# Kernel tuning notes

Hardware: AMD Instinct MI355X
Metric: run time of the kernel (lower is better)

Reference implementation:

```python
import jax, jax.numpy as jnp
import numpy as np

B, T, D_EMB, D_H = 4, 4096, 512, 64


def setup_inputs() -> dict:
    key = jax.random.key(0)
    ks = jax.random.split(key, 7)
    s_in = 1.0 / np.sqrt(D_EMB)
    return {
        "x": jax.random.normal(ks[0], (B, T, D_EMB), jnp.float32),
        "Wq_w": jax.random.normal(ks[1], (D_H, D_EMB), jnp.float32) * s_in,
        "Wq_b": jax.random.normal(ks[2], (D_H,), jnp.float32) * 0.02,
        "Wk_w": jax.random.normal(ks[3], (D_H, D_EMB), jnp.float32) * s_in,
        "Wk_b": jax.random.normal(ks[4], (D_H,), jnp.float32) * 0.02,
        "Wv_w": jax.random.normal(ks[5], (D_H, D_EMB), jnp.float32) * s_in,
        "Wv_b": jax.random.normal(ks[6], (D_H,), jnp.float32) * 0.02,
    }


def reference(x, Wq_w, Wq_b, Wk_w, Wk_b, Wv_w, Wv_b):
    # Q,K,V: [B,T,d_h] via torch.nn.Linear semantics (x @ W.T + b)
    Q = jnp.einsum("btc,hc->bth", x, Wq_w) + Wq_b
    K = jnp.einsum("btc,hc->bth", x, Wk_w) + Wk_b
    V = jnp.einsum("btc,hc->bth", x, Wv_w) + Wv_b
    # raw scores [B,T,T], causal mask, softmax, then post-softmax scale by sqrt(d_h)
    scores = jnp.einsum("bqh,bkh->bqk", Q, K)
    causal = jnp.tril(jnp.ones((T, T), dtype=bool))
    scores = jnp.where(causal, scores, -jnp.inf)
    alpha = jax.nn.softmax(scores, axis=-1) * jnp.sqrt(jnp.float32(D_H))
    return jnp.einsum("bqk,bkh->bqh", alpha, V)
```

## Files before the change

### kernel.cpp

```cpp
#include <hip/hip_runtime.h>
#include <hip/hip_fp16.h>
#include <math.h>

#define B 4
#define T 4096
#define DEMB 512
#define DH 64
#define NSPLIT 16
#define NPTILE 16
#define LOG2E 1.44269504088896340736f

typedef _Float16 f16;
typedef __attribute__((ext_vector_type(4))) _Float16 f16x4;
typedef __attribute__((ext_vector_type(8))) _Float16 f16x8;
typedef __attribute__((ext_vector_type(4))) float f32x4;

__global__ __launch_bounds__(256) void convert_w(
    const float* __restrict__ Wq, const float* __restrict__ Wk,
    const float* __restrict__ Wv, f16* __restrict__ Wf)
{
    const int idx = blockIdx.x * 256 + threadIdx.x;
    const int row = idx >> 9;
    const int k   = idx & 511;
    const float* W = row < 64 ? Wq : (row < 128 ? Wk : Wv);
    Wf[idx] = (f16)W[(row & 63) * DEMB + k];
}

__global__ __launch_bounds__(512) void proj_mfma(
    const float* __restrict__ x, const f16* __restrict__ Wfg,
    const float* __restrict__ bq, const float* __restrict__ bk,
    const float* __restrict__ bv,
    f16* __restrict__ Qf, f16* __restrict__ Kf, f16* __restrict__ Vt)
{
    __shared__ f16 xs[32][136];
    __shared__ f16 Ws[192][136];

    const int tid  = threadIdx.x;
    const int wv   = tid >> 6;
    const int lane = tid & 63;
    const int i16  = lane & 15;
    const int quad = lane >> 4;
    const int rg   = wv >> 2;
    const int nh   = wv & 3;
    const size_t r0 = (size_t)blockIdx.x * 32;

    f32x4 acc[3];
    const f32x4 zero = {0.f, 0.f, 0.f, 0.f};
#pragma unroll
    for (int n = 0; n < 3; ++n) acc[n] = zero;

    for (int cc = 0; cc < DEMB; cc += 128) {
        __syncthreads();
        {
            const int row = tid >> 4, g = tid & 15;
            const float4 a = *(const float4*)(x + (r0 + row) * DEMB + cc + g * 8);
            const float4 b = *(const float4*)(x + (r0 + row) * DEMB + cc + g * 8 + 4);
            f16x8 h = {(f16)a.x, (f16)a.y, (f16)a.z, (f16)a.w,
                       (f16)b.x, (f16)b.y, (f16)b.z, (f16)b.w};
            *(f16x8*)&xs[row][g * 8] = h;
        }
#pragma unroll
        for (int u = 0; u < 6; ++u) {
            const int idx = tid + 512 * u;
            const int row = idx >> 4, g = idx & 15;
            *(f16x8*)&Ws[row][g * 8] =
                *(const f16x8*)(Wfg + (size_t)row * DEMB + cc + g * 8);
        }
        __syncthreads();

#pragma unroll
        for (int kk = 0; kk < 4; ++kk) {
            const f16x8 af = *(const f16x8*)&xs[rg * 16 + i16][kk * 32 + quad * 8];
#pragma unroll
            for (int n = 0; n < 3; ++n) {
                const f16x8 bf = *(const f16x8*)&Ws[(nh * 3 + n) * 16 + i16][kk * 32 + quad * 8];
                acc[n] = __builtin_amdgcn_mfma_f32_16x16x32_f16(af, bf, acc[n], 0, 0, 0);
            }
        }
    }

    const size_t bb = r0 / T;
    const size_t t0 = r0 - bb * T;
#pragma unroll
    for (int n = 0; n < 3; ++n) {
        const int col = (nh * 3 + n) * 16 + i16;
        const int m = col >> 6, h = col & 63;
        const float bias = (m == 0 ? bq : (m == 1 ? bk : bv))[h];
#pragma unroll
        for (int r = 0; r < 4; ++r) {
            const int row = rg * 16 + quad * 4 + r;
            const float v = acc[n][r] + bias;
            const size_t grow = r0 + row;
            if (m == 0)      Qf[grow * DH + h] = (f16)(v * LOG2E);
            else if (m == 1) Kf[grow * DH + h] = (f16)v;
            else             Vt[(bb * DH + h) * T + t0 + row] = (f16)v;
        }
    }
}

__global__ __launch_bounds__(512, 4) void attn_partial(
    const f16* __restrict__ Qf, const f16* __restrict__ Kf,
    const f16* __restrict__ Vt,
    f16* __restrict__ Opart, float* __restrict__ mpart,
    float* __restrict__ lpart)
{
    __shared__ f16 Ks[64][72], Vs[64][72];
    __shared__ f16 Pl[8][16][72];

    const int tid  = threadIdx.x;
    const int wv   = tid >> 6;
    const int lane = tid & 63;
    const int i16  = lane & 15;
    const int quad = lane >> 4;

    const int s    = blockIdx.x & 15;
    const int p    = 15 - ((blockIdx.x >> 4) & 15);
    const int bb   = blockIdx.x >> 8;
    const size_t base = (size_t)bb * T;
    const int row0 = p * 256;
    const int cmax = 4 * p + 3;
    const int rowg0 = row0 + wv * 16;
    const int rowg1 = row0 + (wv + 8) * 16;

    f16x8 qf00, qf01, qf10, qf11;
    {
        const f16* q0 = Qf + (base + rowg0 + i16) * DH;
        const f16* q1 = Qf + (base + rowg1 + i16) * DH;
        qf00 = *(const f16x8*)(q0 + quad * 8);
        qf01 = *(const f16x8*)(q0 + 32 + quad * 8);
        qf10 = *(const f16x8*)(q1 + quad * 8);
        qf11 = *(const f16x8*)(q1 + 32 + quad * 8);
    }

    f32x4 oacc[2][4];
    float mm[2] = {-INFINITY, -INFINITY}, ll[2] = {0.f, 0.f};
    const f32x4 zero = {0.f, 0.f, 0.f, 0.f};
#pragma unroll
    for (int j = 0; j < 2; ++j)
#pragma unroll
        for (int n = 0; n < 4; ++n) oacc[j][n] = zero;

    const int srow = tid >> 3, sg = tid & 7;

    for (int c = s; c <= cmax; c += NSPLIT) {
        const int kb = c << 6;
        __syncthreads();
        *(f16x8*)&Ks[srow][sg * 8] =
            *(const f16x8*)(Kf + (base + kb + srow) * DH + sg * 8);
        *(f16x8*)&Vs[srow][sg * 8] =
            *(const f16x8*)(Vt + ((size_t)bb * DH + srow) * T + kb + sg * 8);
        __syncthreads();

        const bool a0 = kb <= rowg0, a1 = kb <= rowg1;
        if (!a1) continue;

        f32x4 st[2][4];
#pragma unroll
        for (int kt = 0; kt < 4; ++kt) {
            const f16x8 kf0 = *(const f16x8*)&Ks[kt * 16 + i16][quad * 8];
            const f16x8 kf1 = *(const f16x8*)&Ks[kt * 16 + i16][32 + quad * 8];
            if (a0) {
                f32x4 a = __builtin_amdgcn_mfma_f32_16x16x32_f16(kf0, qf00, zero, 0, 0, 0);
                st[0][kt] = __builtin_amdgcn_mfma_f32_16x16x32_f16(kf1, qf01, a, 0, 0, 0);
            }
            {
                f32x4 a = __builtin_amdgcn_mfma_f32_16x16x32_f16(kf0, qf10, zero, 0, 0, 0);
                st[1][kt] = __builtin_amdgcn_mfma_f32_16x16x32_f16(kf1, qf11, a, 0, 0, 0);
            }
        }
        f16x8 pf[2][2];
#pragma unroll
        for (int j = 0; j < 2; ++j) {
            if (j == 0 && !a0) continue;
            const int rowg = j == 0 ? rowg0 : rowg1;
            if (kb + 63 > rowg) {
#pragma unroll
                for (int kt = 0; kt < 4; ++kt)
#pragma unroll
                    for (int r = 0; r < 4; ++r)
                        if (kb + kt * 16 + quad * 4 + r > rowg + i16)
                            st[j][kt][r] = -INFINITY;
            }
            float mx = -INFINITY;
#pragma unroll
            for (int kt = 0; kt < 4; ++kt)
#pragma unroll
                for (int r = 0; r < 4; ++r) mx = fmaxf(mx, st[j][kt][r]);
            mx = fmaxf(mx, __shfl_xor(mx, 16, 64));
            mx = fmaxf(mx, __shfl_xor(mx, 32, 64));
            const float mnew = fmaxf(mm[j], mx);
            const float alpha = exp2f(mm[j] - mnew);
            mm[j] = mnew;
            float sum = 0.f;
#pragma unroll
            for (int kt = 0; kt < 4; ++kt) {
                f16x4 pk;
#pragma unroll
                for (int r = 0; r < 4; ++r) {
                    const f16 pb = (f16)exp2f(st[j][kt][r] - mnew);
                    pk[r] = pb;
                    sum += (float)pb;
                }
                *(f16x4*)&Pl[wv][i16][kt * 16 + quad * 4] = pk;
            }
            sum += __shfl_xor(sum, 16, 64);
            sum += __shfl_xor(sum, 32, 64);
            ll[j] = ll[j] * alpha + sum;
#pragma unroll
            for (int n = 0; n < 4; ++n) oacc[j][n] *= alpha;
            pf[j][0] = *(const f16x8*)&Pl[wv][i16][quad * 8];
            pf[j][1] = *(const f16x8*)&Pl[wv][i16][32 + quad * 8];
        }
#pragma unroll
        for (int mt = 0; mt < 4; ++mt) {
            const f16x8 vf0 = *(const f16x8*)&Vs[mt * 16 + i16][quad * 8];
            const f16x8 vf1 = *(const f16x8*)&Vs[mt * 16 + i16][32 + quad * 8];
            if (a0) {
                oacc[0][mt] = __builtin_amdgcn_mfma_f32_16x16x32_f16(vf0, pf[0][0], oacc[0][mt], 0, 0, 0);
                oacc[0][mt] = __builtin_amdgcn_mfma_f32_16x16x32_f16(vf1, pf[0][1], oacc[0][mt], 0, 0, 0);
            }
            oacc[1][mt] = __builtin_amdgcn_mfma_f32_16x16x32_f16(vf0, pf[1][0], oacc[1][mt], 0, 0, 0);
            oacc[1][mt] = __builtin_amdgcn_mfma_f32_16x16x32_f16(vf1, pf[1][1], oacc[1][mt], 0, 0, 0);
        }
    }

    f16* Ob = Opart + (size_t)blockIdx.x * (256 * 64);
#pragma unroll
    for (int j = 0; j < 2; ++j) {
        const int prow = (wv + 8 * j) * 16 + i16;
#pragma unroll
        for (int mt = 0; mt < 4; ++mt) {
            f16x4 pk = {(f16)oacc[j][mt][0], (f16)oacc[j][mt][1],
                        (f16)oacc[j][mt][2], (f16)oacc[j][mt][3]};
            *(f16x4*)&Ob[prow * 64 + mt * 16 + quad * 4] = pk;
        }
        if (quad == 0) {
            mpart[(size_t)blockIdx.x * 256 + prow] = mm[j];
            lpart[(size_t)blockIdx.x * 256 + prow] = ll[j];
        }
    }
}

__global__ __launch_bounds__(256) void attn_combine(
    const f16* __restrict__ Opart, const float* __restrict__ mpart,
    const float* __restrict__ lpart, float* __restrict__ O)
{
    __shared__ float ws[16][NSPLIT];
    __shared__ float scl[16];

    const int tid = threadIdx.x;
    const int sub = blockIdx.x & 15;
    const int p   = (blockIdx.x >> 4) & 15;
    const int bb  = blockIdx.x >> 8;
    const size_t pb0 = (size_t)bb * 256 + (15 - p) * 16;
    const int nact = min(NSPLIT, 4 * p + 4);
    const int r0c  = sub * 16;

    if (tid < 16) {
        const int row = r0c + tid;
        float m[NSPLIT];
        float M = -INFINITY;
        for (int q = 0; q < nact; ++q) {
            m[q] = mpart[(pb0 + q) * 256 + row];
            M = fmaxf(M, m[q]);
        }
        float L = 0.f;
        for (int q = 0; q < nact; ++q) {
            const float w = exp2f(m[q] - M);
            ws[tid][q] = w;
            L += w * lpart[(pb0 + q) * 256 + row];
        }
        scl[tid] = 8.0f / L;
    }
    __syncthreads();

    const int rowl = tid >> 4;
    const int c4   = tid & 15;
    const int row  = r0c + rowl;
    float a0 = 0.f, a1 = 0.f, a2 = 0.f, a3 = 0.f;
    for (int q = 0; q < nact; ++q) {
        const f16x4 v = *(const f16x4*)&Opart[(pb0 + q) * (256 * 64) + row * 64 + c4 * 4];
        const float w = ws[rowl][q];
        a0 += w * (float)v[0]; a1 += w * (float)v[1];
        a2 += w * (float)v[2]; a3 += w * (float)v[3];
    }
    const float s = scl[rowl];
    const float4 o = {a0 * s, a1 * s, a2 * s, a3 * s};
    *(float4*)&O[((size_t)bb * T + p * 256 + row) * DH + c4 * 4] = o;
}

extern "C" void kernel_launch(void* const* d_in, const int* in_sizes, int n_in,
                              void* d_out, int out_size, void* d_ws, size_t ws_size,
                              hipStream_t stream) {
    const float* x  = (const float*)d_in[0];
    const float* Wq = (const float*)d_in[1];
    const float* bq = (const float*)d_in[2];
    const float* Wk = (const float*)d_in[3];
    const float* bk = (const float*)d_in[4];
    const float* Wv = (const float*)d_in[5];
    const float* bv = (const float*)d_in[6];

    const size_t N  = (size_t)B * T * DH;
    f16* Qf = (f16*)d_ws;
    f16* Kf = Qf + N;
    f16* Vt = Kf + N;
    f16* Wf = Vt + N;
    f16* Opart = Wf + (size_t)192 * DEMB;
    float* mpart = (float*)(Opart + (size_t)1024 * 256 * 64);
    float* lpart = mpart + (size_t)1024 * 256;

    convert_w<<<dim3(192 * DEMB / 256), dim3(256), 0, stream>>>(Wq, Wk, Wv, Wf);
    proj_mfma<<<dim3(B * T / 32), dim3(512), 0, stream>>>(
        x, Wf, bq, bk, bv, Qf, Kf, Vt);
    attn_partial<<<dim3(B * NPTILE * NSPLIT), dim3(512), 0, stream>>>(
        Qf, Kf, Vt, Opart, mpart, lpart);
    attn_combine<<<dim3(B * NPTILE * 16), dim3(256), 0, stream>>>(
        Opart, mpart, lpart, (float*)d_out);
}
```

Baseline: 134.7 us.

## Halve split-K count, double-buffer K/V tiles, prefetch projection loads, use fast exp2

The attention split count drops from 16 to 8, and blocks with no work now exit early. K/V tiles are register-prefetched into a double-buffered shared-memory tile, which removes one barrier per iteration. The projection kernel prefetches the next x/W chunk into registers during the MFMAs, and exp2f is replaced by the hardware exp2 builtin. The fewer splits shrink partial-output traffic and combine work, at the cost of less parallelism and more serial work per block for long causal rows. The occupancy hint on attn_partial is also removed.

Result: no change. 132.6 us (-1.5%).

```diff
diff --git a/kernel.cpp b/kernel.cpp
--- a/kernel.cpp
+++ b/kernel.cpp
@@ -6,7 +6,7 @@
 #define T 4096
 #define DEMB 512
 #define DH 64
-#define NSPLIT 16
+#define NSPLIT 8
 #define NPTILE 16
 #define LOG2E 1.44269504088896340736f
 
@@ -14,6 +14,10 @@
 typedef __attribute__((ext_vector_type(4))) _Float16 f16x4;
 typedef __attribute__((ext_vector_type(8))) _Float16 f16x8;
 typedef __attribute__((ext_vector_type(4))) float f32x4;
+
+__device__ __forceinline__ float fexp2(float x) {
+    return __builtin_amdgcn_exp2f(x);
+}
 
 __global__ __launch_bounds__(256) void convert_w(
     const float* __restrict__ Wq, const float* __restrict__ Wk,
@@ -44,6 +48,21 @@
     const int nh   = wv & 3;
     const size_t r0 = (size_t)blockIdx.x * 32;
 
+    const int xrow = tid >> 4, xg = tid & 15;
+    float4 xa, xb;
+    f16x8 wpre[6];
+
+    {
+        xa = *(const float4*)(x + (r0 + xrow) * DEMB + xg * 8);
+        xb = *(const float4*)(x + (r0 + xrow) * DEMB + xg * 8 + 4);
+#pragma unroll
+        for (int u = 0; u < 6; ++u) {
+            const int idx = tid + 512 * u;
+            const int row = idx >> 4, g = idx & 15;
+            wpre[u] = *(const f16x8*)(Wfg + (size_t)row * DEMB + g * 8);
+        }
+    }
+
     f32x4 acc[3];
     const f32x4 zero = {0.f, 0.f, 0.f, 0.f};
 #pragma unroll
@@ -52,21 +71,29 @@
     for (int cc = 0; cc < DEMB; cc += 128) {
         __syncthreads();
         {
-            const int row = tid >> 4, g = tid & 15;
-            const float4 a = *(const float4*)(x + (r0 + row) * DEMB + cc + g * 8);
-            const float4 b = *(const float4*)(x + (r0 + row) * DEMB + cc + g * 8 + 4);
-            f16x8 h = {(f16)a.x, (f16)a.y, (f16)a.z, (f16)a.w,
-                       (f16)b.x, (f16)b.y, (f16)b.z, (f16)b.w};
-            *(f16x8*)&xs[row][g * 8] = h;
+            f16x8 h = {(f16)xa.x, (f16)xa.y, (f16)xa.z, (f16)xa.w,
+                       (f16)xb.x, (f16)xb.y, (f16)xb.z, (f16)xb.w};
+            *(f16x8*)&xs[xrow][xg * 8] = h;
         }
 #pragma unroll
         for (int u = 0; u < 6; ++u) {
             const int idx = tid + 512 * u;
             const int row = idx >> 4, g = idx & 15;
-            *(f16x8*)&Ws[row][g * 8] =
-                *(const f16x8*)(Wfg + (size_t)row * DEMB + cc + g * 8);
+            *(f16x8*)&Ws[row][g * 8] = wpre[u];
         }
         __syncthreads();
+
+        if (cc + 128 < DEMB) {
+            const int cn = cc + 128;
+            xa = *(const float4*)(x + (r0 + xrow) * DEMB + cn + xg * 8);
+            xb = *(const float4*)(x + (r0 + xrow) * DEMB + cn + xg * 8 + 4);
+#pragma unroll
+            for (int u = 0; u < 6; ++u) {
+                const int idx = tid + 512 * u;
+                const int row = idx >> 4, g = idx & 15;
+                wpre[u] = *(const f16x8*)(Wfg + (size_t)row * DEMB + cn + g * 8);
+            }
+        }
 
 #pragma unroll
         for (int kk = 0; kk < 4; ++kk) {
@@ -98,13 +125,13 @@
     }
 }
 
-__global__ __launch_bounds__(512, 4) void attn_partial(
+__global__ __launch_bounds__(512) void attn_partial(
     const f16* __restrict__ Qf, const f16* __restrict__ Kf,
     const f16* __restrict__ Vt,
     f16* __restrict__ Opart, float* __restrict__ mpart,
     float* __restrict__ lpart)
 {
-    __shared__ f16 Ks[64][72], Vs[64][72];
+    __shared__ f16 Ks[2][64][72], Vs[2][64][72];
     __shared__ f16 Pl[8][16][72];
 
     const int tid  = threadIdx.x;
@@ -113,12 +140,13 @@
     const int i16  = lane & 15;
     const int quad = lane >> 4;
 
-    const int s    = blockIdx.x & 15;
-    const int p    = 15 - ((blockIdx.x >> 4) & 15);
-    const int bb   = blockIdx.x >> 8;
+    const int s    = blockIdx.x & 7;
+    const int p    = 15 - ((blockIdx.x >> 3) & 15);
+    const int bb   = blockIdx.x >> 7;
     const size_t base = (size_t)bb * T;
     const int row0 = p * 256;
     const int cmax = 4 * p + 3;
+    if (s > cmax) return;
     const int rowg0 = row0 + wv * 16;
     const int rowg1 = row0 + (wv + 8) * 16;
 
@@ -141,87 +169,99 @@
         for (int n = 0; n < 4; ++n) oacc[j][n] = zero;
 
     const int srow = tid >> 3, sg = tid & 7;
-
+    f16x8 kpre, vpre;
+    {
+        const int kb = s << 6;
+        kpre = *(const f16x8*)(Kf + (base + kb + srow) * DH + sg * 8);
+        vpre = *(const f16x8*)(Vt + ((size_t)bb * DH + srow) * T + kb + sg * 8);
+    }
+
+    int buf = 0;
     for (int c = s; c <= cmax; c += NSPLIT) {
+        *(f16x8*)&Ks[buf][srow][sg * 8] = kpre;
+        *(f16x8*)&Vs[buf][srow][sg * 8] = vpre;
+        __syncthreads();
+
+        const int cn = c + NSPLIT;
+        if (cn <= cmax) {
+            const int kbn = cn << 6;
+            kpre = *(const f16x8*)(Kf + (base + kbn + srow) * DH + sg * 8);
+            vpre = *(const f16x8*)(Vt + ((size_t)bb * DH + srow) * T + kbn + sg * 8);
+        }
+
         const int kb = c << 6;
-        __syncthreads();
-        *(f16x8*)&Ks[srow][sg * 8] =
-            *(const f16x8*)(Kf + (base + kb + srow) * DH + sg * 8);
-        *(f16x8*)&Vs[srow][sg * 8] =
-            *(const f16x8*)(Vt + ((size_t)bb * DH + srow) * T + kb + sg * 8);
-        __syncthreads();
-
         const bool a0 = kb <= rowg0, a1 = kb <= rowg1;
-        if (!a1) continue;
-
-        f32x4 st[2][4];
-#pragma unroll
-        for (int kt = 0; kt < 4; ++kt) {
-            const f16x8 kf0 = *(const f16x8*)&Ks[kt * 16 + i16][quad * 8];
-            const f16x8 kf1 = *(const f16x8*)&Ks[kt * 16 + i16][32 + quad * 8];
-            if (a0) {
-                f32x4 a = __builtin_amdgcn_mfma_f32_16x16x32_f16(kf0, qf00, zero, 0, 0, 0);
-                st[0][kt] = __builtin_amdgcn_mfma_f32_16x16x32_f16(kf1, qf01, a, 0, 0, 0);
-            }
-            {
-                f32x4 a = __builtin_amdgcn_mfma_f32_16x16x32_f16(kf0, qf10, zero, 0, 0, 0);
-                st[1][kt] = __builtin_amdgcn_mfma_f32_16x16x32_f16(kf1, qf11, a, 0, 0, 0);
-            }
-        }
-        f16x8 pf[2][2];
-#pragma unroll
-        for (int j = 0; j < 2; ++j) {
-            if (j == 0 && !a0) continue;
-            const int rowg = j == 0 ? rowg0 : rowg1;
-            if (kb + 63 > rowg) {
+        if (a1) {
+            f32x4 st[2][4];
+#pragma unroll
+            for (int kt = 0; kt < 4; ++kt) {
+                const f16x8 kf0 = *(const f16x8*)&Ks[buf][kt * 16 + i16][quad * 8];
+                const f16x8 kf1 = *(const f16x8*)&Ks[buf][kt * 16 + i16][32 + quad * 8];
+                if (a0) {
+                    f32x4 a = __builtin_amdgcn_mfma_f32_16x16x32_f16(kf0, qf00, zero, 0, 0, 0);
+                    st[0][kt] = __builtin_amdgcn_mfma_f32_16x16x32_f16(kf1, qf01, a, 0, 0, 0);
+                }
+                {
+                    f32x4 a = __builtin_amdgcn_mfma_f32_16x16x32_f16(kf0, qf10, zero, 0, 0, 0);
+                    st[1][kt] = __builtin_amdgcn_mfma_f32_16x16x32_f16(kf1, qf11, a, 0, 0, 0);
+                }
+            }
+            f16x8 pf[2][2];
+#pragma unroll
+            for (int j = 0; j < 2; ++j) {
+                if (j == 0 && !a0) continue;
+                const int rowg = j == 0 ? rowg0 : rowg1;
+                if (kb + 63 > rowg) {
+#pragma unroll
+                    for (int kt = 0; kt < 4; ++kt)
+#pragma unroll
+                        for (int r = 0; r < 4; ++r)
+                            if (kb + kt * 16 + quad * 4 + r > rowg + i16)
+                                st[j][kt][r] = -INFINITY;
+                }
+                float mx = -INFINITY;
 #pragma unroll
                 for (int kt = 0; kt < 4; ++kt)
 #pragma unroll
-                    for (int r = 0; r < 4; ++r)
-                        if (kb + kt * 16 + quad * 4 + r > rowg + i16)
-                            st[j][kt][r] = -INFINITY;
-            }
-            float mx = -INFINITY;
-#pragma unroll
-            for (int kt = 0; kt < 4; ++kt)
-#pragma unroll
-                for (int r = 0; r < 4; ++r) mx = fmaxf(mx, st[j][kt][r]);
-            mx = fmaxf(mx, __shfl_xor(mx, 16, 64));
-            mx = fmaxf(mx, __shfl_xor(mx, 32, 64));
-            const float mnew = fmaxf(mm[j], mx);
-            const float alpha = exp2f(mm[j] - mnew);
-            mm[j] = mnew;
-            float sum = 0.f;
-#pragma unroll
-            for (int kt = 0; kt < 4; ++kt) {
-                f16x4 pk;
-#pragma unroll
-                for (int r = 0; r < 4; ++r) {
-                    const f16 pb = (f16)exp2f(st[j][kt][r] - mnew);
-                    pk[r] = pb;
-                    sum += (float)pb;
-                }
-                *(f16x4*)&Pl[wv][i16][kt * 16 + quad * 4] = pk;
-            }
-            sum += __shfl_xor(sum, 16, 64);
-            sum += __shfl_xor(sum, 32, 64);
-            ll[j] = ll[j] * alpha + sum;
-#pragma unroll
-            for (int n = 0; n < 4; ++n) oacc[j][n] *= alpha;
-            pf[j][0] = *(const f16x8*)&Pl[wv][i16][quad * 8];
-            pf[j][1] = *(const f16x8*)&Pl[wv][i16][32 + quad * 8];
-        }
-#pragma unroll
-        for (int mt = 0; mt < 4; ++mt) {
-            const f16x8 vf0 = *(const f16x8*)&Vs[mt * 16 + i16][quad * 8];
-            const f16x8 vf1 = *(const f16x8*)&Vs[mt * 16 + i16][32 + quad * 8];
-            if (a0) {
-                oacc[0][mt] = __builtin_amdgcn_mfma_f32_16x16x32_f16(vf0, pf[0][0], oacc[0][mt], 0, 0, 0);
-                oacc[0][mt] = __builtin_amdgcn_mfma_f32_16x16x32_f16(vf1, pf[0][1], oacc[0][mt], 0, 0, 0);
-            }
-            oacc[1][mt] = __builtin_amdgcn_mfma_f32_16x16x32_f16(vf0, pf[1][0], oacc[1][mt], 0, 0, 0);
-            oacc[1][mt] = __builtin_amdgcn_mfma_f32_16x16x32_f16(vf1, pf[1][1], oacc[1][mt], 0, 0, 0);
-        }
+                    for (int r = 0; r < 4; ++r) mx = fmaxf(mx, st[j][kt][r]);
+                mx = fmaxf(mx, __shfl_xor(mx, 16, 64));
+                mx = fmaxf(mx, __shfl_xor(mx, 32, 64));
+                const float mnew = fmaxf(mm[j], mx);
+                const float alpha = fexp2(mm[j] - mnew);
+                mm[j] = mnew;
+                float sum = 0.f;
+#pragma unroll
+                for (int kt = 0; kt < 4; ++kt) {
+                    f16x4 pk;
+#pragma unroll
+                    for (int r = 0; r < 4; ++r) {
+                        const f16 pb = (f16)fexp2(st[j][kt][r] - mnew);
+                        pk[r] = pb;
+                        sum += (float)pb;
+                    }
+                    *(f16x4*)&Pl[wv][i16][kt * 16 + quad * 4] = pk;
+                }
+                sum += __shfl_xor(sum, 16, 64);
+                sum += __shfl_xor(sum, 32, 64);
+                ll[j] = ll[j] * alpha + sum;
+#pragma unroll
+                for (int n = 0; n < 4; ++n) oacc[j][n] *= alpha;
+                pf[j][0] = *(const f16x8*)&Pl[wv][i16][quad * 8];
+                pf[j][1] = *(const f16x8*)&Pl[wv][i16][32 + quad * 8];
+            }
+#pragma unroll
+            for (int mt = 0; mt < 4; ++mt) {
+                const f16x8 vf0 = *(const f16x8*)&Vs[buf][mt * 16 + i16][quad * 8];
+                const f16x8 vf1 = *(const f16x8*)&Vs[buf][mt * 16 + i16][32 + quad * 8];
+                if (a0) {
+                    oacc[0][mt] = __builtin_amdgcn_mfma_f32_16x16x32_f16(vf0, pf[0][0], oacc[0][mt], 0, 0, 0);
+                    oacc[0][mt] = __builtin_amdgcn_mfma_f32_16x16x32_f16(vf1, pf[0][1], oacc[0][mt], 0, 0, 0);
+                }
+                oacc[1][mt] = __builtin_amdgcn_mfma_f32_16x16x32_f16(vf0, pf[1][0], oacc[1][mt], 0, 0, 0);
+                oacc[1][mt] = __builtin_amdgcn_mfma_f32_16x16x32_f16(vf1, pf[1][1], oacc[1][mt], 0, 0, 0);
+            }
+        }
+        buf ^= 1;
     }
 
     f16* Ob = Opart + (size_t)blockIdx.x * (256 * 64);
@@ -252,7 +292,7 @@
     const int sub = blockIdx.x & 15;
     const int p   = (blockIdx.x >> 4) & 15;
     const int bb  = blockIdx.x >> 8;
-    const size_t pb0 = (size_t)bb * 256 + (15 - p) * 16;
+    const size_t pb0 = (size_t)bb * 128 + (15 - p) * NSPLIT;
     const int nact = min(NSPLIT, 4 * p + 4);
     const int r0c  = sub * 16;
 
@@ -266,7 +306,7 @@
         }
         float L = 0.f;
         for (int q = 0; q < nact; ++q) {
-            const float w = exp2f(m[q] - M);
+            const float w = fexp2(m[q] - M);
             ws[tid][q] = w;
             L += w * lpart[(pb0 + q) * 256 + row];
         }
@@ -306,8 +346,8 @@
     f16* Vt = Kf + N;
     f16* Wf = Vt + N;
     f16* Opart = Wf + (size_t)192 * DEMB;
-    float* mpart = (float*)(Opart + (size_t)1024 * 256 * 64);
-    float* lpart = mpart + (size_t)1024 * 256;
+    float* mpart = (float*)(Opart + (size_t)512 * 256 * 64);
+    float* lpart = mpart + (size_t)512 * 256;
 
     convert_w<<<dim3(192 * DEMB / 256), dim3(256), 0, stream>>>(Wq, Wk, Wv, Wf);
     proj_mfma<<<dim3(B * T / 32), dim3(512), 0, stream>>>(
```
